# Optimization experiments

Measured on AMD Instinct MI355X. Metric: run time of the kernel, lower is better.

Reference implementation:

```python
import jax, jax.numpy as jnp
import numpy as np

HIDDEN = 256
TOPK = 16
SINK_BLOCKS = 5
TAU = 1.0
SOFT_ALPHA = 8.0
LN_EPS = 1e-5


def setup_inputs() -> dict:
    key = jax.random.key(0)
    ks = jax.random.split(key, 8)
    B, T, QD, KD, J = 2, 1024, 1024, 1024, 64
    H = HIDDEN
    H3 = 3 * H
    s = 0.02
    return {
        "Q": jax.random.normal(ks[0], (B, T, QD), dtype=jnp.float32),
        "K": jax.random.normal(ks[1], (B, J, KD), dtype=jnp.float32),
        "Wq": jax.random.normal(ks[2], (H, QD), dtype=jnp.float32) * s,
        "Wk": jax.random.normal(ks[3], (H, KD), dtype=jnp.float32) * s,
        "ln_g": jnp.ones((H3,), dtype=jnp.float32),
        "ln_b": jnp.zeros((H3,), dtype=jnp.float32),
        "Wu": jax.random.normal(ks[4], (H, H3), dtype=jnp.float32) * s,
        "bu": jnp.zeros((H,), dtype=jnp.float32),
        "Wv": jax.random.normal(ks[5], (H, H3), dtype=jnp.float32) * s,
        "bv": jnp.zeros((H,), dtype=jnp.float32),
        "Wo": jax.random.normal(ks[6], (1, H), dtype=jnp.float32) * s,
        "bo": jnp.zeros((1,), dtype=jnp.float32),
        "chunk_len": 16,
        "L_ctx": 1024,
    }


def _forward(Q, K, Wq, Wk, ln_g, ln_b, Wu, bu, Wv, bv, Wo, bo, chunk_len, L_ctx):
    B, T, _ = Q.shape
    J = K.shape[1]
    # ---- GatedScorer ----
    q = jnp.einsum('btd,hd->bth', Q, Wq)  # (B,T,H)
    k = jnp.einsum('bjd,hd->bjh', K, Wk)  # (B,J,H)
    H = q.shape[-1]
    qb = jnp.broadcast_to(q[:, :, None, :], (B, T, J, H))
    kb = jnp.broadcast_to(k[:, None, :, :], (B, T, J, H))
    x = jnp.concatenate([qb, kb, qb * kb], axis=-1)  # (B,T,J,3H)
    mu = jnp.mean(x, axis=-1, keepdims=True)
    var = jnp.mean((x - mu) ** 2, axis=-1, keepdims=True)
    x = (x - mu) / jnp.sqrt(var + LN_EPS) * ln_g + ln_b
    U = jnp.einsum('btjc,hc->btjh', x, Wu) + bu
    V = jnp.einsum('btjc,hc->btjh', x, Wv) + bv
    Z = U * jax.nn.gelu(V, approximate=False)
    logits = jnp.einsum('btjh,oh->btjo', Z, Wo)[..., 0] + bo[0]  # (B,T,J)

    # ---- top-k chunk selection (deterministic path, use_learnable_k=False) ----
    sink = int(min(max(0, SINK_BLOCKS), J))
    J_tail = J - sink
    topk_main = max(min(J, TOPK) - sink, 0)
    logits_tail = logits[..., sink:]  # (B,T,J_tail)
    causal = jnp.arange(J_tail)[None, :] <= jnp.arange(T)[:, None]  # tril(T,J_tail)
    masked = jnp.where(causal[None], logits_tail, -jnp.inf)
    _, idx_tail = jax.lax.top_k(masked, topk_main)
    idx_tail = idx_tail + sink
    sink_idx = jnp.broadcast_to(jnp.arange(sink)[None, None, :], (B, T, sink))
    idx = jnp.concatenate([sink_idx, idx_tail], axis=-1)  # (B,T,sink+topk_main)

    # ---- soft warmup weights ----
    w_soft = jax.nn.softmax(logits / TAU, axis=-1)  # (B,T,J)

    # ---- build_block_bias_from_topk ----
    num_chunks = (L_ctx + chunk_len - 1) // chunk_len
    sel = jnp.zeros((B, T, num_chunks), dtype=bool)
    sel = sel.at[jnp.arange(B)[:, None, None], jnp.arange(T)[None, :, None], idx].set(True)
    token_chunk = jnp.clip(jnp.arange(L_ctx) // chunk_len, 0, num_chunks - 1)  # (L_ctx,)
    sel_tok = jnp.take(sel, token_chunk, axis=-1)  # (B,T,L_ctx)
    per_chunk_bias = -SOFT_ALPHA * (1.0 - w_soft)  # (B,T,J)
    bias = jnp.take(per_chunk_bias, token_chunk, axis=-1)  # (B,T,L_ctx)
    bias = jnp.where(sel_tok, 0.0, bias)
    tri = jnp.arange(L_ctx)[None, :] > jnp.arange(T)[:, None]  # triu(T,L_ctx, diag=1)
    bias = jnp.where(tri[None], -jnp.inf, bias)
    return logits, bias


def reference(Q, K, Wq, Wk, ln_g, ln_b, Wu, bu, Wv, bv, Wo, bo, chunk_len, L_ctx):
    return _forward(Q, K, Wq, Wk, ln_g, ln_b, Wu, bu, Wv, bv, Wo, bo, chunk_len, L_ctx)
```

## Files before the change

kernel.cpp:

```cpp
#include <hip/hip_runtime.h>
#include <hip/hip_bf16.h>
#include <math.h>

#define H3 768

#define OFF_Q     0u
#define OFF_K     524288u
#define OFF_UVK   557056u
#define OFF_SQ    622592u
#define OFF_SQ2   624768u
#define OFF_WGU   626944u
#define OFF_WGV   627200u
#define OFF_CU    627456u
#define OFF_CV    627712u

#define BO_UVQ   0u
#define BO_WQF   1048576u
#define BO_WKF   1310720u
#define BO_BPK   1572864u
#define BO_WQBF  1703936u
#define BO_WKBF  1835008u

typedef __attribute__((ext_vector_type(8))) short bf16x8;
typedef __attribute__((ext_vector_type(4))) float f32x4;

__device__ __forceinline__ float bf2f(short s) {
    return __uint_as_float(((unsigned)(unsigned short)s) << 16);
}
union bfu { __hip_bfloat162 h; short2 s; };
__device__ __forceinline__ void split2(float a, float b, short* hi2, short* lo2) {
    bfu h; h.h = __float22bfloat162_rn(float2{a, b});
    float fa = bf2f(h.s.x), fb = bf2f(h.s.y);
    bfu l; l.h = __float22bfloat162_rn(float2{a - fa, b - fb});
    hi2[0] = h.s.x; hi2[1] = h.s.y;
    lo2[0] = l.s.x; lo2[1] = l.s.y;
}
__device__ __forceinline__ void split8(const float* v, bf16x8* vh, bf16x8* vl) {
    short h2[2], l2[2];
#pragma unroll
    for (int i = 0; i < 4; i++) {
        split2(v[2 * i], v[2 * i + 1], h2, l2);
        (*vh)[2 * i] = h2[0]; (*vh)[2 * i + 1] = h2[1];
        (*vl)[2 * i] = l2[0]; (*vl)[2 * i + 1] = l2[1];
    }
}

__device__ __forceinline__ float gelu_fast(float v) {
    float ar = v * 0.70710678118654752440f;
    float a = fabsf(ar);
    float t = __builtin_amdgcn_rcpf(fmaf(0.3275911f, a, 1.0f));
    float p = fmaf(fmaf(fmaf(fmaf(1.061405429f, t, -1.453152027f), t,
                             1.421413741f), t, -0.284496736f), t, 0.254829592f) * t;
    float e = __expf(-ar * ar);
    float er = fmaf(-p, e, 1.0f);
    er = copysignf(er, ar);
    return 0.5f * v * (1.0f + er);
}

__device__ __forceinline__ float wave_reduce_add(float v) {
#pragma unroll
    for (int off = 32; off > 0; off >>= 1) v += __shfl_xor(v, off, 64);
    return v;
}

__global__ __launch_bounds__(256) void prep(const float* __restrict__ Wq,
                                            const float* __restrict__ Wk,
                                            const float* __restrict__ Wu,
                                            const float* __restrict__ Wv,
                                            const float* __restrict__ g,
                                            const float* __restrict__ lb,
                                            const float* __restrict__ bu,
                                            const float* __restrict__ bv,
                                            float* __restrict__ ws,
                                            float* __restrict__ bsc) {
    int tid = threadIdx.x;
    int bid = blockIdx.x;
    if (bid >= 512) {
        ws[(bid - 512) * 256 + tid] = 0.0f;
        return;
    }
    if (bid < 64) {
        int h = bid * 4 + (tid >> 6);
        int lane = tid & 63;
        float su = 0.f, sv = 0.f, tu = 0.f, tv = 0.f;
#pragma unroll
        for (int i = 0; i < 12; i++) {
            int c = lane + 64 * i;
            float gg = g[c], bb = lb[c];
            float wu = Wu[h * H3 + c], wv = Wv[h * H3 + c];
            su += wu * gg; sv += wv * gg; tu += wu * bb; tv += wv * bb;
        }
        su = wave_reduce_add(su); sv = wave_reduce_add(sv);
        tu = wave_reduce_add(tu); tv = wave_reduce_add(tv);
        if (lane == 0) {
            ws[OFF_WGU + h] = su; ws[OFF_WGV + h] = sv;
            ws[OFF_CU + h] = tu + bu[h]; ws[OFF_CV + h] = tv + bv[h];
        }
        return;
    }
    float v8[8];
    bf16x8 vh, vl;
    if (bid < 320) {
        const float* W; bf16x8* dst;
        int idx;
        if (bid < 192) { idx = (bid - 64) * 256 + tid; W = Wq; dst = (bf16x8*)(bsc + BO_WQF); }
        else { idx = (bid - 192) * 256 + tid; W = Wk; dst = (bf16x8*)(bsc + BO_WKF); }
        int n = idx >> 7, k8 = idx & 127;
        const float* src = W + (size_t)n * 1024 + k8 * 8;
        *(float4*)&v8[0] = *(const float4*)src;
        *(float4*)&v8[4] = *(const float4*)(src + 4);
        split8(v8, &vh, &vl);
        int kc = k8 >> 2, grp = k8 & 3, lane = grp * 16 + (n & 15), ntg = n >> 4;
        size_t s0 = ((size_t)(kc * 16 + ntg) * 2) * 64 + lane;
        dst[s0] = vh; dst[s0 + 64] = vl;
        return;
    }
    int idx, c0;
    bf16x8* dst;
    int n;
    if (bid < 384) {
        idx = (bid - 320) * 256 + tid;
        n = idx >> 5; c0 = (idx & 31) * 8;
        dst = (bf16x8*)(bsc + BO_WQBF);
    } else if (bid < 448) {
        idx = (bid - 384) * 256 + tid;
        n = idx >> 5; c0 = 256 + (idx & 31) * 8;
        dst = (bf16x8*)(bsc + BO_WKBF);
    } else {
        idx = (bid - 448) * 256 + tid;
        n = idx >> 5; c0 = 512 + (idx & 31) * 8;
        dst = (bf16x8*)(bsc + BO_BPK);
    }
    int h, uv;
    if (bid < 448) { uv = (n < 256) ? 0 : 1; h = (n < 256) ? n : n - 256; }
    else {
        int ntg0 = n >> 4, cc = n & 15;
        uv = ntg0 & 1;
        h = ((ntg0 >> 3) << 6) | (((ntg0 >> 1) & 3) << 4) | cc;
    }
    const float* W = uv ? Wv : Wu;
#pragma unroll
    for (int i = 0; i < 8; i++) v8[i] = W[(size_t)h * H3 + c0 + i] * g[c0 + i];
    split8(v8, &vh, &vl);
    int k8 = (c0 & 255) >> 3;
    int kc = k8 >> 2, grp = k8 & 3, lane = grp * 16 + (n & 15), ntg = n >> 4;
    size_t s0 = ((size_t)(kc * 32 + ntg) * 2) * 64 + lane;
    dst[s0] = vh; dst[s0 + 64] = vl;
}

__global__ __launch_bounds__(256) void proj_mfma(const float* __restrict__ Q,
                                                 const float* __restrict__ Kin,
                                                 const float* __restrict__ bsc,
                                                 float* __restrict__ ws) {
    __shared__ __align__(16) short Ah[2][32 * 40], Al[2][32 * 40];
    int tid = threadIdx.x, bx = blockIdx.x, by = blockIdx.y, ks = blockIdx.z;
    const float* A; float* C; const bf16x8* BF;
    if (by < 64) {
        A = Q + (size_t)by * 32 * 1024;
        C = ws + OFF_Q + (size_t)by * 32 * 256;
        BF = (const bf16x8*)(bsc + BO_WQF);
    } else {
        A = Kin + (size_t)(by - 64) * 32 * 1024;
        C = ws + OFF_K + (size_t)(by - 64) * 32 * 256;
        BF = (const bf16x8*)(bsc + BO_WKF);
    }
    int w = tid >> 6, l = tid & 63, c15 = l & 15, grp = l >> 4;
    int mt = w & 1, np = w >> 1;
    int srow = tid >> 3, scol = (tid & 7) * 4;
    const float* arow = A + (size_t)srow * 1024 + ks * 512 + scol;
    f32x4 acc[2];
    acc[0] = (f32x4){0.f, 0.f, 0.f, 0.f};
    acc[1] = (f32x4){0.f, 0.f, 0.f, 0.f};
    float4 a4 = *(const float4*)&arow[0];
    for (int kc = 0; kc < 16; kc++) {
        int pb = kc & 1;
        short h4[4], l4[4];
        split2(a4.x, a4.y, &h4[0], &l4[0]);
        split2(a4.z, a4.w, &h4[2], &l4[2]);
        int ao = srow * 40 + scol;
        *(short4*)&Ah[pb][ao] = *(short4*)&h4[0];
        *(short4*)&Al[pb][ao] = *(short4*)&l4[0];
        if (kc < 15) a4 = *(const float4*)&arow[(kc + 1) * 32];
        __syncthreads();
        int fo = (mt * 16 + c15) * 40 + grp * 8;
        bf16x8 afh = *(const bf16x8*)&Ah[pb][fo];
        bf16x8 afl = *(const bf16x8*)&Al[pb][fo];
        int kcg = ks * 16 + kc;
        bf16x8 bh[2], bl[2];
#pragma unroll
        for (int i = 0; i < 2; i++) {
            int ntg = bx * 4 + 2 * np + i;
            size_t fi = ((size_t)(kcg * 16 + ntg) * 2) * 64 + l;
            bh[i] = BF[fi]; bl[i] = BF[fi + 64];
        }
#pragma unroll
        for (int i = 0; i < 2; i++)
            acc[i] = __builtin_amdgcn_mfma_f32_16x16x32_bf16(afl, bh[i], acc[i], 0, 0, 0);
#pragma unroll
        for (int i = 0; i < 2; i++)
            acc[i] = __builtin_amdgcn_mfma_f32_16x16x32_bf16(afh, bl[i], acc[i], 0, 0, 0);
#pragma unroll
        for (int i = 0; i < 2; i++)
            acc[i] = __builtin_amdgcn_mfma_f32_16x16x32_bf16(afh, bh[i], acc[i], 0, 0, 0);
    }
#pragma unroll
    for (int r = 0; r < 4; r++) {
        int rloc = mt * 16 + grp * 4 + r;
#pragma unroll
        for (int i = 0; i < 2; i++)
            atomicAdd(&C[(size_t)rloc * 256 + bx * 64 + (2 * np + i) * 16 + c15], acc[i][r]);
    }
}

__global__ __launch_bounds__(256) void uv_mfma(float* __restrict__ ws,
                                               float* __restrict__ bsc) {
    __shared__ __align__(16) short Ah[64 * 40], Al[64 * 40];
    int tid = threadIdx.x, bx = blockIdx.x, by = blockIdx.y;
    const float* A; float* C; const bf16x8* BF; int sbase;
    if (by < 32) {
        A = ws + OFF_Q + (size_t)by * 64 * 256;
        C = bsc + BO_UVQ + (size_t)by * 64 * 512;
        BF = (const bf16x8*)(bsc + BO_WQBF);
        sbase = by * 64;
    } else {
        A = ws + OFF_K + (size_t)(by - 32) * 64 * 256;
        C = ws + OFF_UVK + (size_t)(by - 32) * 64 * 512;
        BF = (const bf16x8*)(bsc + BO_WKBF);
        sbase = 2048 + (by - 32) * 64;
    }
    int w = tid >> 6, l = tid & 63, c15 = l & 15, grp = l >> 4;
    int srow = tid >> 2, scol = (tid & 3) * 8;
    f32x4 acc[4];
#pragma unroll
    for (int nt = 0; nt < 4; nt++) acc[nt] = (f32x4){0.f, 0.f, 0.f, 0.f};
    float s1 = 0.f, s2 = 0.f;
    for (int kc = 0; kc < 8; kc++) {
        float v8[8];
        const float* src = &A[(size_t)srow * 256 + kc * 32 + scol];
        *(float4*)&v8[0] = *(const float4*)src;
        *(float4*)&v8[4] = *(const float4*)(src + 4);
        if (bx == 0) {
#pragma unroll
            for (int i = 0; i < 8; i++) { s1 += v8[i]; s2 = fmaf(v8[i], v8[i], s2); }
        }
        bf16x8 vh, vl;
        split8(v8, &vh, &vl);
        int ao = srow * 40 + scol;
        *(bf16x8*)&Ah[ao] = vh;
        *(bf16x8*)&Al[ao] = vl;
        __syncthreads();
        int fo = (w * 16 + c15) * 40 + grp * 8;
        bf16x8 afh = *(const bf16x8*)&Ah[fo];
        bf16x8 afl = *(const bf16x8*)&Al[fo];
        bf16x8 bh[4], bl[4];
#pragma unroll
        for (int nt = 0; nt < 4; nt++) {
            int ntg = bx * 4 + nt;
            size_t fi = ((size_t)(kc * 32 + ntg) * 2) * 64 + l;
            bh[nt] = BF[fi]; bl[nt] = BF[fi + 64];
        }
#pragma unroll
        for (int nt = 0; nt < 4; nt++)
            acc[nt] = __builtin_amdgcn_mfma_f32_16x16x32_bf16(afl, bh[nt], acc[nt], 0, 0, 0);
#pragma unroll
        for (int nt = 0; nt < 4; nt++)
            acc[nt] = __builtin_amdgcn_mfma_f32_16x16x32_bf16(afh, bl[nt], acc[nt], 0, 0, 0);
#pragma unroll
        for (int nt = 0; nt < 4; nt++)
            acc[nt] = __builtin_amdgcn_mfma_f32_16x16x32_bf16(afh, bh[nt], acc[nt], 0, 0, 0);
        __syncthreads();
    }
    if (bx == 0) {
        s1 += __shfl_xor(s1, 1, 64); s1 += __shfl_xor(s1, 2, 64);
        s2 += __shfl_xor(s2, 1, 64); s2 += __shfl_xor(s2, 2, 64);
        if ((tid & 3) == 0) {
            ws[OFF_SQ + sbase + srow] = s1;
            ws[OFF_SQ2 + sbase + srow] = s2;
        }
    }
#pragma unroll
    for (int nt = 0; nt < 4; nt++)
#pragma unroll
        for (int r = 0; r < 4; r++)
            C[(size_t)(w * 16 + grp * 4 + r) * 512 + bx * 64 + nt * 16 + c15] = acc[nt][r];
}

__global__ __launch_bounds__(256, 3) void main_mfma(const float* __restrict__ ws,
                                                    const float* __restrict__ bsc,
                                                    const float* __restrict__ Wo,
                                                    const float* __restrict__ bo,
                                                    float* __restrict__ logits) {
    __shared__ float kk[256];
    __shared__ __align__(16) short Ah[8][32 * 32];
    __shared__ __align__(16) short Al[8][32 * 32];
    __shared__ float mu_s[32], inv_s[32];
    __shared__ float part_s[4][32];
    int tid = threadIdx.x;
    int bidf = blockIdx.x;
    int xcd = bidf & 7;
    int m = bidf >> 3;
    int ti = (xcd << 2) | (m & 3);
    int j = (m >> 2) & 63;
    int b = bidf >> 11;
    int t0 = ti << 5;
    int bj = (b << 6) | j;
    int rot8 = xcd;
    kk[tid] = ws[OFF_K + bj * 256 + tid];
    int w = tid >> 6, l = tid & 63, c15 = l & 15, grp = l >> 4;
    int srow = tid >> 3, scol = (tid & 7) * 4;
    const float* qrow = ws + OFF_Q + (size_t)((b << 10) + t0 + srow) * 256 + scol;
    const bf16x8* bpk = (const bf16x8*)(bsc + BO_BPK);
    const float* UVQ = bsc + BO_UVQ;
    f32x4 acc[2][8];
#pragma unroll
    for (int mt = 0; mt < 2; mt++)
#pragma unroll
        for (int nt = 0; nt < 8; nt++) acc[mt][nt] = (f32x4){0.f, 0.f, 0.f, 0.f};
    float s1 = 0.f, s2 = 0.f;
    int ntg0 = w * 8;
    __syncthreads();
#pragma unroll
    for (int kc = 0; kc < 8; kc++) {
        float4 q4 = *(const float4*)&qrow[kc * 32];
        float4 k4 = *(const float4*)&kk[kc * 32 + scol];
        float a0 = q4.x * k4.x;
        float a1 = q4.y * k4.y;
        float a2 = q4.z * k4.z;
        float a3 = q4.w * k4.w;
        s1 += (a0 + a1) + (a2 + a3);
        s2 = fmaf(a0, a0, s2); s2 = fmaf(a1, a1, s2);
        s2 = fmaf(a2, a2, s2); s2 = fmaf(a3, a3, s2);
        short h2[2], l2[2];
        short4 vh, vl;
        split2(a0, a1, h2, l2);
        vh.x = h2[0]; vh.y = h2[1]; vl.x = l2[0]; vl.y = l2[1];
        split2(a2, a3, h2, l2);
        vh.z = h2[0]; vh.w = h2[1]; vl.z = l2[0]; vl.w = l2[1];
        int ao = srow * 32 + scol;
        *(short4*)&Ah[kc][ao] = vh;
        *(short4*)&Al[kc][ao] = vl;
    }
    s1 += __shfl_xor(s1, 1, 64); s1 += __shfl_xor(s1, 2, 64); s1 += __shfl_xor(s1, 4, 64);
    s2 += __shfl_xor(s2, 1, 64); s2 += __shfl_xor(s2, 2, 64); s2 += __shfl_xor(s2, 4, 64);
    if ((tid & 7) == 0) {
        int row = (b << 10) + t0 + srow;
        float sq = s1 + ws[OFF_SQ + row] + ws[OFF_SQ + 2048 + bj];
        float sq2 = s2 + ws[OFF_SQ2 + row] + ws[OFF_SQ2 + 2048 + bj];
        float muv = sq * (1.0f / 768.0f);
        float ex2 = sq2 * (1.0f / 768.0f);
        mu_s[srow] = muv;
        inv_s[srow] = 1.0f / sqrtf(ex2 - muv * muv + 1e-5f);
    }
    __syncthreads();
#pragma unroll
    for (int ii = 0; ii < 8; ii++) {
        int kcg = (ii + rot8) & 7;
        bf16x8 afh[2], afl[2];
#pragma unroll
        for (int mt = 0; mt < 2; mt++) {
            int ao = (mt * 16 + c15) * 32 + grp * 8;
            afh[mt] = *(const bf16x8*)&Ah[kcg][ao];
            afl[mt] = *(const bf16x8*)&Al[kcg][ao];
        }
        const bf16x8* bpc = bpk + ((size_t)(kcg * 32 + ntg0) * 2) * 64 + l;
#pragma unroll
        for (int np = 0; np < 4; np++) {
            bf16x8 bh0 = bpc[(size_t)(2 * np) * 128];
            bf16x8 bl0 = bpc[(size_t)(2 * np) * 128 + 64];
            bf16x8 bh1 = bpc[(size_t)(2 * np + 1) * 128];
            bf16x8 bl1 = bpc[(size_t)(2 * np + 1) * 128 + 64];
#pragma unroll
            for (int mt = 0; mt < 2; mt++)
                acc[mt][2 * np] = __builtin_amdgcn_mfma_f32_16x16x32_bf16(afl[mt], bh0, acc[mt][2 * np], 0, 0, 0);
#pragma unroll
            for (int mt = 0; mt < 2; mt++)
                acc[mt][2 * np + 1] = __builtin_amdgcn_mfma_f32_16x16x32_bf16(afl[mt], bh1, acc[mt][2 * np + 1], 0, 0, 0);
#pragma unroll
            for (int mt = 0; mt < 2; mt++)
                acc[mt][2 * np] = __builtin_amdgcn_mfma_f32_16x16x32_bf16(afh[mt], bl0, acc[mt][2 * np], 0, 0, 0);
#pragma unroll
            for (int mt = 0; mt < 2; mt++)
                acc[mt][2 * np + 1] = __builtin_amdgcn_mfma_f32_16x16x32_bf16(afh[mt], bl1, acc[mt][2 * np + 1], 0, 0, 0);
#pragma unroll
            for (int mt = 0; mt < 2; mt++)
                acc[mt][2 * np] = __builtin_amdgcn_mfma_f32_16x16x32_bf16(afh[mt], bh0, acc[mt][2 * np], 0, 0, 0);
#pragma unroll
            for (int mt = 0; mt < 2; mt++)
                acc[mt][2 * np + 1] = __builtin_amdgcn_mfma_f32_16x16x32_bf16(afh[mt], bh1, acc[mt][2 * np + 1], 0, 0, 0);
        }
    }
    float wgu_r[4], wgv_r[4], cu_r[4], cv_r[4], wo_r[4], uk_r[4], vk_r[4];
    int h4[4];
#pragma unroll
    for (int a = 0; a < 4; a++) {
        int h = (w << 6) | (a << 4) | c15;
        h4[a] = h;
        wgu_r[a] = ws[OFF_WGU + h]; wgv_r[a] = ws[OFF_WGV + h];
        cu_r[a] = ws[OFF_CU + h]; cv_r[a] = ws[OFF_CV + h];
        wo_r[a] = Wo[h];
        uk_r[a] = ws[OFF_UVK + (size_t)bj * 512 + h];
        vk_r[a] = ws[OFF_UVK + (size_t)bj * 512 + 256 + h];
    }
#pragma unroll
    for (int mt = 0; mt < 2; mt++) {
#pragma unroll
        for (int r4 = 0; r4 < 4; r4++) {
            int r = mt * 16 + grp * 4 + r4;
            int row = (b << 10) + t0 + r;
            float muv = mu_s[r], invv = inv_s[r];
            const float* uvq = UVQ + (size_t)row * 512;
            float part = 0.f;
#pragma unroll
            for (int a = 0; a < 4; a++) {
                float U = invv * (acc[mt][2 * a][r4] + uvq[h4[a]] + uk_r[a] - muv * wgu_r[a]) + cu_r[a];
                float V = invv * (acc[mt][2 * a + 1][r4] + uvq[256 + h4[a]] + vk_r[a] - muv * wgv_r[a]) + cv_r[a];
                part = fmaf(wo_r[a] * U, gelu_fast(V), part);
            }
            part += __shfl_xor(part, 1, 64);
            part += __shfl_xor(part, 2, 64);
            part += __shfl_xor(part, 4, 64);
            part += __shfl_xor(part, 8, 64);
            if (c15 == 0) part_s[w][r] = part;
        }
    }
    __syncthreads();
    if (tid < 32) {
        float v = bo[0] + part_s[0][tid] + part_s[1][tid] + part_s[2][tid] + part_s[3][tid];
        logits[(size_t)((b << 10) + t0 + tid) * 64 + j] = v;
    }
}

__global__ __launch_bounds__(256) void topk_bias(const float* __restrict__ logits,
                                                 float* __restrict__ bias,
                                                 const int* __restrict__ p_cl,
                                                 const int* __restrict__ p_L) {
    int wv = threadIdx.x >> 6, lane = threadIdx.x & 63;
    int row = blockIdx.x * 4 + wv;
    int t = row & 1023;
    __shared__ float pcb[4][64];
    float L = logits[(size_t)row * 64 + lane];
    float mx = L;
#pragma unroll
    for (int off = 32; off > 0; off >>= 1) mx = fmaxf(mx, __shfl_xor(mx, off, 64));
    float e = expf(L - mx);
    float s = wave_reduce_add(e);
    pcb[wv][lane] = -8.0f * (1.0f - e / s);
    bool valid = (lane >= 5) && ((lane - 5) <= t);
    float val = (lane >= 5) ? (valid ? L : -INFINITY) : -INFINITY;
    int idv = (lane >= 5) ? lane : (1 << 28);
    unsigned long long selmask = 0x1Full;
    for (int it = 0; it < 11; it++) {
        float bv = val; int bi = idv;
#pragma unroll
        for (int off = 32; off > 0; off >>= 1) {
            float ov = __shfl_xor(bv, off, 64);
            int oi = __shfl_xor(bi, off, 64);
            if (ov > bv || (ov == bv && oi < bi)) { bv = ov; bi = oi; }
        }
        selmask |= 1ull << bi;
        if (lane == bi) { val = -INFINITY; idv = (1 << 27); }
    }
    int clen = p_cl[0], Lctx = p_L[0];
    int nch1 = (Lctx + clen - 1) / clen - 1;
    bool p2 = (clen & (clen - 1)) == 0;
    int sh = 31 - __clz(clen);
    float* brow = bias + (size_t)row * Lctx;
    if ((Lctx & 3) == 0) {
        float4* brow4 = (float4*)brow;
        for (int q = lane; q < (Lctx >> 2); q += 64) {
            float o[4];
#pragma unroll
            for (int i = 0; i < 4; i++) {
                int ll = 4 * q + i;
                unsigned cq = p2 ? ((unsigned)ll >> sh) : ((unsigned)ll / (unsigned)clen);
                int c = min(min(cq, (unsigned)nch1), 63u);
                float v;
                if (ll > t) v = -1e30f;
                else if ((selmask >> c) & 1ull) v = 0.0f;
                else v = pcb[wv][c];
                o[i] = v;
            }
            brow4[q] = *(float4*)&o[0];
        }
    } else {
        for (int ll = lane; ll < Lctx; ll += 64) {
            unsigned cq = p2 ? ((unsigned)ll >> sh) : ((unsigned)ll / (unsigned)clen);
            int c = min(min(cq, (unsigned)nch1), 63u);
            float v;
            if (ll > t) v = -1e30f;
            else if ((selmask >> c) & 1ull) v = 0.0f;
            else v = pcb[wv][c];
            brow[ll] = v;
        }
    }
}

extern "C" void kernel_launch(void* const* d_in, const int* in_sizes, int n_in,
                              void* d_out, int out_size, void* d_ws, size_t ws_size,
                              hipStream_t stream) {
    const float* Q   = (const float*)d_in[0];
    const float* Kin = (const float*)d_in[1];
    const float* Wq  = (const float*)d_in[2];
    const float* Wk  = (const float*)d_in[3];
    const float* g   = (const float*)d_in[4];
    const float* lb  = (const float*)d_in[5];
    const float* Wu  = (const float*)d_in[6];
    const float* bu  = (const float*)d_in[7];
    const float* Wv  = (const float*)d_in[8];
    const float* bv  = (const float*)d_in[9];
    const float* Wo  = (const float*)d_in[10];
    const float* bo  = (const float*)d_in[11];
    const int* p_cl  = (const int*)d_in[12];
    const int* p_L   = (const int*)d_in[13];
    float* ws = (float*)d_ws;
    float* logits = (float*)d_out;
    float* bias = (float*)d_out + (size_t)2 * 1024 * 64;

    prep<<<2688, 256, 0, stream>>>(Wq, Wk, Wu, Wv, g, lb, bu, bv, ws, bias);
    proj_mfma<<<dim3(4, 68, 2), 256, 0, stream>>>(Q, Kin, bias, ws);
    uv_mfma<<<dim3(8, 34), 256, 0, stream>>>(ws, bias);
    main_mfma<<<4096, 256, 0, stream>>>(ws, bias, Wo, bo, logits);
    topk_bias<<<512, 256, 0, stream>>>(logits, bias, p_cl, p_L);
}
```

Before: 232.3 us.

## Restructure gated scorer MFMA loop per output tile with prefetch and swizzled LDS

Reorders the fused scorer GEMM so each wave handles one 16-column U/V output tile at a time over all K chunks, then runs the GELU epilogue right away. Only 4 accumulator tiles stay live instead of 16, which cuts register pressure. B-fragment loads are software-prefetched one step ahead, the LDS A tiles are XOR-swizzled to avoid bank conflicts, and s_setprio is raised around the MFMA bursts. The cost is that A fragments are reloaded from LDS four times instead of once, and the epilogue's global UVQ loads are spread across the loop.

```diff
diff --git a/kernel.cpp b/kernel.cpp
--- a/kernel.cpp
+++ b/kernel.cpp
@@ -311,14 +311,22 @@
     const float* qrow = ws + OFF_Q + (size_t)((b << 10) + t0 + srow) * 256 + scol;
     const bf16x8* bpk = (const bf16x8*)(bsc + BO_BPK);
     const float* UVQ = bsc + BO_UVQ;
-    f32x4 acc[2][8];
-#pragma unroll
-    for (int mt = 0; mt < 2; mt++)
-#pragma unroll
-        for (int nt = 0; nt < 8; nt++) acc[mt][nt] = (f32x4){0.f, 0.f, 0.f, 0.f};
+    int ntg0 = w * 8;
+    float wgu_r[4], wgv_r[4], cu_r[4], cv_r[4], wo_r[4], uk_r[4], vk_r[4];
+#pragma unroll
+    for (int a = 0; a < 4; a++) {
+        int h = (w << 6) | (a << 4) | c15;
+        wgu_r[a] = ws[OFF_WGU + h]; wgv_r[a] = ws[OFF_WGV + h];
+        cu_r[a] = ws[OFF_CU + h]; cv_r[a] = ws[OFF_CV + h];
+        wo_r[a] = Wo[h];
+        uk_r[a] = ws[OFF_UVK + (size_t)bj * 512 + h];
+        vk_r[a] = ws[OFF_UVK + (size_t)bj * 512 + 256 + h];
+    }
     float s1 = 0.f, s2 = 0.f;
-    int ntg0 = w * 8;
     __syncthreads();
+    int slot = scol >> 3;
+    int sw = slot ^ (srow & 3) ^ ((srow >> 2) & 3);
+    int ao = srow * 32 + (sw << 3) + (scol & 7);
 #pragma unroll
     for (int kc = 0; kc < 8; kc++) {
         float4 q4 = *(const float4*)&qrow[kc * 32];
@@ -336,7 +344,6 @@
         vh.x = h2[0]; vh.y = h2[1]; vl.x = l2[0]; vl.y = l2[1];
         split2(a2, a3, h2, l2);
         vh.z = h2[0]; vh.w = h2[1]; vl.z = l2[0]; vl.w = l2[1];
-        int ao = srow * 32 + scol;
         *(short4*)&Ah[kc][ao] = vh;
         *(short4*)&Al[kc][ao] = vl;
     }
@@ -352,75 +359,90 @@
         inv_s[srow] = 1.0f / sqrtf(ex2 - muv * muv + 1e-5f);
     }
     __syncthreads();
-#pragma unroll
-    for (int ii = 0; ii < 8; ii++) {
-        int kcg = (ii + rot8) & 7;
-        bf16x8 afh[2], afl[2];
-#pragma unroll
-        for (int mt = 0; mt < 2; mt++) {
-            int ao = (mt * 16 + c15) * 32 + grp * 8;
-            afh[mt] = *(const bf16x8*)&Ah[kcg][ao];
-            afl[mt] = *(const bf16x8*)&Al[kcg][ao];
-        }
-        const bf16x8* bpc = bpk + ((size_t)(kcg * 32 + ntg0) * 2) * 64 + l;
-#pragma unroll
-        for (int np = 0; np < 4; np++) {
-            bf16x8 bh0 = bpc[(size_t)(2 * np) * 128];
-            bf16x8 bl0 = bpc[(size_t)(2 * np) * 128 + 64];
-            bf16x8 bh1 = bpc[(size_t)(2 * np + 1) * 128];
-            bf16x8 bl1 = bpc[(size_t)(2 * np + 1) * 128 + 64];
-#pragma unroll
-            for (int mt = 0; mt < 2; mt++)
-                acc[mt][2 * np] = __builtin_amdgcn_mfma_f32_16x16x32_bf16(afl[mt], bh0, acc[mt][2 * np], 0, 0, 0);
-#pragma unroll
-            for (int mt = 0; mt < 2; mt++)
-                acc[mt][2 * np + 1] = __builtin_amdgcn_mfma_f32_16x16x32_bf16(afl[mt], bh1, acc[mt][2 * np + 1], 0, 0, 0);
-#pragma unroll
-            for (int mt = 0; mt < 2; mt++)
-                acc[mt][2 * np] = __builtin_amdgcn_mfma_f32_16x16x32_bf16(afh[mt], bl0, acc[mt][2 * np], 0, 0, 0);
-#pragma unroll
-            for (int mt = 0; mt < 2; mt++)
-                acc[mt][2 * np + 1] = __builtin_amdgcn_mfma_f32_16x16x32_bf16(afh[mt], bl1, acc[mt][2 * np + 1], 0, 0, 0);
-#pragma unroll
-            for (int mt = 0; mt < 2; mt++)
-                acc[mt][2 * np] = __builtin_amdgcn_mfma_f32_16x16x32_bf16(afh[mt], bh0, acc[mt][2 * np], 0, 0, 0);
-#pragma unroll
-            for (int mt = 0; mt < 2; mt++)
-                acc[mt][2 * np + 1] = __builtin_amdgcn_mfma_f32_16x16x32_bf16(afh[mt], bh1, acc[mt][2 * np + 1], 0, 0, 0);
-        }
-    }
-    float wgu_r[4], wgv_r[4], cu_r[4], cv_r[4], wo_r[4], uk_r[4], vk_r[4];
-    int h4[4];
-#pragma unroll
-    for (int a = 0; a < 4; a++) {
-        int h = (w << 6) | (a << 4) | c15;
-        h4[a] = h;
-        wgu_r[a] = ws[OFF_WGU + h]; wgv_r[a] = ws[OFF_WGV + h];
-        cu_r[a] = ws[OFF_CU + h]; cv_r[a] = ws[OFF_CV + h];
-        wo_r[a] = Wo[h];
-        uk_r[a] = ws[OFF_UVK + (size_t)bj * 512 + h];
-        vk_r[a] = ws[OFF_UVK + (size_t)bj * 512 + 256 + h];
-    }
-#pragma unroll
-    for (int mt = 0; mt < 2; mt++) {
+    float mu_r[2][4], inv_r[2][4];
+#pragma unroll
+    for (int mt = 0; mt < 2; mt++)
 #pragma unroll
         for (int r4 = 0; r4 < 4; r4++) {
             int r = mt * 16 + grp * 4 + r4;
-            int row = (b << 10) + t0 + r;
-            float muv = mu_s[r], invv = inv_s[r];
-            const float* uvq = UVQ + (size_t)row * 512;
-            float part = 0.f;
-#pragma unroll
-            for (int a = 0; a < 4; a++) {
-                float U = invv * (acc[mt][2 * a][r4] + uvq[h4[a]] + uk_r[a] - muv * wgu_r[a]) + cu_r[a];
-                float V = invv * (acc[mt][2 * a + 1][r4] + uvq[256 + h4[a]] + vk_r[a] - muv * wgv_r[a]) + cv_r[a];
-                part = fmaf(wo_r[a] * U, gelu_fast(V), part);
+            mu_r[mt][r4] = mu_s[r];
+            inv_r[mt][r4] = inv_s[r];
+        }
+    int rx = (c15 & 3) ^ ((c15 >> 2) & 3);
+    int aro0 = c15 * 32 + ((grp ^ rx) << 3);
+    int aro1 = (16 + c15) * 32 + ((grp ^ rx) << 3);
+    const bf16x8* bpkL = bpk + l;
+    float part[2][4];
+#pragma unroll
+    for (int mt = 0; mt < 2; mt++)
+#pragma unroll
+        for (int r4 = 0; r4 < 4; r4++) part[mt][r4] = 0.f;
+    bf16x8 bh0, bl0, bh1, bl1;
+    {
+        const bf16x8* bp0 = bpkL + ((size_t)(rot8 * 32 + ntg0) * 2) * 64;
+        bh0 = bp0[0]; bl0 = bp0[64]; bh1 = bp0[128]; bl1 = bp0[192];
+    }
+#pragma unroll
+    for (int a = 0; a < 4; a++) {
+        f32x4 aU[2], aV[2];
+        aU[0] = (f32x4){0.f, 0.f, 0.f, 0.f}; aU[1] = (f32x4){0.f, 0.f, 0.f, 0.f};
+        aV[0] = (f32x4){0.f, 0.f, 0.f, 0.f}; aV[1] = (f32x4){0.f, 0.f, 0.f, 0.f};
+#pragma unroll
+        for (int ii = 0; ii < 8; ii++) {
+            int kcg = (ii + rot8) & 7;
+            bf16x8 nh0 = bh0, nl0 = bl0, nh1 = bh1, nl1 = bl1;
+            if (ii < 7) {
+                int kn = (ii + 1 + rot8) & 7;
+                const bf16x8* bpn = bpkL + ((size_t)(kn * 32 + ntg0 + 2 * a) * 2) * 64;
+                nh0 = bpn[0]; nl0 = bpn[64]; nh1 = bpn[128]; nl1 = bpn[192];
+            } else if (a < 3) {
+                const bf16x8* bpn = bpkL + ((size_t)(rot8 * 32 + ntg0 + 2 * (a + 1)) * 2) * 64;
+                nh0 = bpn[0]; nl0 = bpn[64]; nh1 = bpn[128]; nl1 = bpn[192];
             }
-            part += __shfl_xor(part, 1, 64);
-            part += __shfl_xor(part, 2, 64);
-            part += __shfl_xor(part, 4, 64);
-            part += __shfl_xor(part, 8, 64);
-            if (c15 == 0) part_s[w][r] = part;
+            bf16x8 afh0 = *(const bf16x8*)&Ah[kcg][aro0];
+            bf16x8 afl0 = *(const bf16x8*)&Al[kcg][aro0];
+            bf16x8 afh1 = *(const bf16x8*)&Ah[kcg][aro1];
+            bf16x8 afl1 = *(const bf16x8*)&Al[kcg][aro1];
+            __builtin_amdgcn_s_setprio(1);
+            aU[0] = __builtin_amdgcn_mfma_f32_16x16x32_bf16(afl0, bh0, aU[0], 0, 0, 0);
+            aU[1] = __builtin_amdgcn_mfma_f32_16x16x32_bf16(afl1, bh0, aU[1], 0, 0, 0);
+            aV[0] = __builtin_amdgcn_mfma_f32_16x16x32_bf16(afl0, bh1, aV[0], 0, 0, 0);
+            aV[1] = __builtin_amdgcn_mfma_f32_16x16x32_bf16(afl1, bh1, aV[1], 0, 0, 0);
+            aU[0] = __builtin_amdgcn_mfma_f32_16x16x32_bf16(afh0, bl0, aU[0], 0, 0, 0);
+            aU[1] = __builtin_amdgcn_mfma_f32_16x16x32_bf16(afh1, bl0, aU[1], 0, 0, 0);
+            aV[0] = __builtin_amdgcn_mfma_f32_16x16x32_bf16(afh0, bl1, aV[0], 0, 0, 0);
+            aV[1] = __builtin_amdgcn_mfma_f32_16x16x32_bf16(afh1, bl1, aV[1], 0, 0, 0);
+            aU[0] = __builtin_amdgcn_mfma_f32_16x16x32_bf16(afh0, bh0, aU[0], 0, 0, 0);
+            aU[1] = __builtin_amdgcn_mfma_f32_16x16x32_bf16(afh1, bh0, aU[1], 0, 0, 0);
+            aV[0] = __builtin_amdgcn_mfma_f32_16x16x32_bf16(afh0, bh1, aV[0], 0, 0, 0);
+            aV[1] = __builtin_amdgcn_mfma_f32_16x16x32_bf16(afh1, bh1, aV[1], 0, 0, 0);
+            __builtin_amdgcn_s_setprio(0);
+            bh0 = nh0; bl0 = nl0; bh1 = nh1; bl1 = nl1;
+        }
+        int h = (w << 6) | (a << 4) | c15;
+#pragma unroll
+        for (int mt = 0; mt < 2; mt++) {
+#pragma unroll
+            for (int r4 = 0; r4 < 4; r4++) {
+                int row = (b << 10) + t0 + mt * 16 + grp * 4 + r4;
+                const float* uvq = UVQ + (size_t)row * 512;
+                float muv = mu_r[mt][r4], invv = inv_r[mt][r4];
+                float U = invv * (aU[mt][r4] + uvq[h] + uk_r[a] - muv * wgu_r[a]) + cu_r[a];
+                float V = invv * (aV[mt][r4] + uvq[256 + h] + vk_r[a] - muv * wgv_r[a]) + cv_r[a];
+                part[mt][r4] = fmaf(wo_r[a] * U, gelu_fast(V), part[mt][r4]);
+            }
+        }
+    }
+#pragma unroll
+    for (int mt = 0; mt < 2; mt++) {
+#pragma unroll
+        for (int r4 = 0; r4 < 4; r4++) {
+            float p = part[mt][r4];
+            p += __shfl_xor(p, 1, 64);
+            p += __shfl_xor(p, 2, 64);
+            p += __shfl_xor(p, 4, 64);
+            p += __shfl_xor(p, 8, 64);
+            if (c15 == 0) part_s[w][mt * 16 + grp * 4 + r4] = p;
         }
     }
     __syncthreads();
```

Result: slower. 316.7 us (+36.3%).
